# Kernel tuning notes

Measured on AMD Instinct MI355X. Metric: run time of the kernel, lower is better.

The kernel has to match this reference:

```python
import jax, jax.numpy as jnp
import numpy as np

ARRAY_SIZE = 128   # crossbar rows
CBITS = 4          # psum ADC bits
LEV = 2 ** (CBITS - 1)
ALPHA = ARRAY_SIZE / LEV   # psum quant step
EPS = 1e-5

# ---- binary activation / weight quant with STE (hardtanh grad) ----
@jax.custom_vjp
def ste_sign(x):
    return jnp.where(x >= 0, 1.0, -1.0).astype(x.dtype)

def _sign_fwd(x):
    return ste_sign(x), x

def _sign_bwd(x, g):
    return (g * (jnp.abs(x) <= 1.0).astype(g.dtype),)

ste_sign.defvjp(_sign_fwd, _sign_bwd)

# ---- psum (partial-sum) quantization: cbits-level ADC over each crossbar array ----
@jax.custom_vjp
def psum_quant(p):
    return jnp.clip(jnp.round(p / ALPHA), -LEV, LEV - 1) * ALPHA

def _pq_fwd(p):
    return psum_quant(p), p

def _pq_bwd(p, g):
    return (g * (jnp.abs(p) <= ARRAY_SIZE).astype(g.dtype),)

psum_quant.defvjp(_pq_fwd, _pq_bwd)

# ---- layers ----
def bn(x, p):
    g, b, m, v = p  # each [C]
    sh = (1, -1) + (1,) * (x.ndim - 2)
    return (x - m.reshape(sh)) * (g.reshape(sh) / jnp.sqrt(v.reshape(sh) + EPS)) + b.reshape(sh)

def maxpool2(x):
    return jax.lax.reduce_window(x, -jnp.inf, jax.lax.max, (1, 1, 2, 2), (1, 1, 2, 2), 'VALID')

def conv_same(x, w):
    return jax.lax.conv_general_dilated(x, w, (1, 1), 'SAME')

def psum_conv(x, w):
    # crossbar-mapped conv: input channels split into groups of arraySize//(kh*kw),
    # each group conv'd separately, psum-quantized (ADC), then accumulated.
    O, Cin, kh, kw = w.shape
    chunk = max(1, ARRAY_SIZE // (kh * kw))
    G = -(-Cin // chunk)
    pad = G * chunk - Cin
    xp = jnp.pad(x, ((0, 0), (0, pad), (0, 0), (0, 0)))
    wp = jnp.pad(w, ((0, 0), (0, pad), (0, 0), (0, 0)))
    B, _, H, W = x.shape
    xg = xp.reshape(B, G, chunk, H, W).transpose(1, 0, 2, 3, 4)   # [G,B,c,H,W]
    wg = wp.reshape(O, G, chunk, kh, kw).transpose(1, 0, 2, 3, 4)  # [G,O,c,kh,kw]
    ps = jax.vmap(conv_same)(xg, wg)                               # [G,B,O,H,W]
    return psum_quant(ps).sum(0)

def psum_linear(x, w):
    # x [B,D], w [O,D]; D divisible by ARRAY_SIZE
    B, D = x.shape
    O = w.shape[0]
    G = D // ARRAY_SIZE
    ps = jnp.einsum('bgc,ogc->gbo', x.reshape(B, G, ARRAY_SIZE), w.reshape(O, G, ARRAY_SIZE))
    return psum_quant(ps).sum(0)


def setup_inputs() -> dict:
    key = jax.random.key(0)
    ks = iter(jax.random.split(key, 64))
    def nrm(shape, s=0.05):
        return jax.random.normal(next(ks), shape, jnp.float32) * s
    def bnp(C):
        return jnp.stack([jax.random.uniform(next(ks), (C,), jnp.float32) + 0.5,
                          nrm((C,), 0.1), nrm((C,), 0.1),
                          jax.random.uniform(next(ks), (C,), jnp.float32) + 0.5])
    return dict(
        x=jax.random.normal(next(ks), (64, 3, 32, 32), jnp.float32),
        conv0_w=nrm((128, 3, 3, 3)), bn0=bnp(128),
        w1=nrm((128, 128, 3, 3)), bn1=bnp(128),
        w2=nrm((256, 128, 3, 3)), bn2=bnp(256),
        w3=nrm((256, 256, 3, 3)), bn3=bnp(256),
        w4=nrm((512, 256, 3, 3)), bn4=bnp(512),
        w5=nrm((512, 512, 3, 3)), bn5=bnp(512),
        fc1_w=nrm((1024, 8192)), bnf1=bnp(1024),
        fc2_w=nrm((1024, 1024)), bnf2=bnp(1024),
        out_w=nrm((10, 1024)), out_b=nrm((10,)), bnout=bnp(10),
    )


def reference(x, conv0_w, bn0, w1, bn1, w2, bn2, w3, bn3, w4, bn4, w5, bn5,
              fc1_w, bnf1, fc2_w, bnf2, out_w, out_b, bnout):
    h = conv_same(x, conv0_w)                       # full-precision first conv
    h = ste_sign(bn(h, bn0))
    h = psum_conv(h, ste_sign(w1)); h = maxpool2(h); h = ste_sign(bn(h, bn1))
    h = psum_conv(h, ste_sign(w2)); h = ste_sign(bn(h, bn2))
    h = psum_conv(h, ste_sign(w3)); h = maxpool2(h); h = ste_sign(bn(h, bn3))
    h = psum_conv(h, ste_sign(w4)); h = ste_sign(bn(h, bn4))
    h = psum_conv(h, ste_sign(w5)); h = maxpool2(h); h = ste_sign(bn(h, bn5))
    h = h.reshape(h.shape[0], -1)                   # [B, 8192]
    h = ste_sign(bn(psum_linear(h, ste_sign(fc1_w)), bnf1))
    h = bn(psum_linear(h, ste_sign(fc2_w)), bnf2)   # abits=32 -> identity nonlinear
    h = h @ out_w.T + out_b
    return bn(h, bnout)
```

## Files before the change

### kernel.cpp

```cpp
#include <hip/hip_runtime.h>
#include <cstdint>
#include <cstddef>

using bf16x8 = __attribute__((ext_vector_type(8))) short;
using f32x4  = __attribute__((ext_vector_type(4))) float;
using u32x4  = __attribute__((ext_vector_type(4))) unsigned int;

#define DI __device__ __forceinline__

DI float pq3(float a) {
    return fminf(rintf(a), 7.f);
}
DI float pq16(float ps) {
    return fminf(rintf(ps * 0.0625f), 7.f) * 16.f;
}

DI float bnv(float x, float g, float b, float m, float v) {
    return (x - m) * (g / sqrtf(v + 1e-5f)) + b;
}

DI unsigned short sgn_bf16(float v) {
    return (v >= 0.f) ? (unsigned short)0x3F80 : (unsigned short)0xBF80;
}

__global__ __launch_bounds__(256)
void k_conv0(const float* __restrict__ x, const float* __restrict__ w,
             const float* __restrict__ bnp, unsigned short* __restrict__ out) {
    __shared__ float sX[3][3][36];
    const int b = blockIdx.x >> 5, y = blockIdx.x & 31;
    const int tid = threadIdx.x;
    const int o = tid & 127, xc = tid >> 7;

    for (int i = tid; i < 3 * 3 * 36; i += 256) {
        int col = i % 36, rr = (i / 36) % 3, c = i / 108;
        int gy = y + rr - 1, gx = col - 1;
        float v = 0.f;
        if ((unsigned)gy < 32u && (unsigned)gx < 32u)
            v = x[((b * 3 + c) * 32 + gy) * 32 + gx];
        sX[c][rr][col] = v;
    }
    float wr[27];
    const float* wp = w + o * 27;
    #pragma unroll
    for (int t = 0; t < 27; ++t) wr[t] = wp[t];
    __syncthreads();

    const float bg = bnp[o], bb = bnp[128 + o], bm = bnp[256 + o], bv = bnp[384 + o];
    unsigned short* op = out + ((size_t)(b * 32 + y) * 32) * 128 + o;

    #pragma unroll
    for (int q = 0; q < 4; ++q) {
        float acc0 = 0.f, acc1 = 0.f, acc2 = 0.f, acc3 = 0.f;
        const int X0 = xc * 16 + q * 4;
        #pragma unroll
        for (int c = 0; c < 3; ++c)
            #pragma unroll
            for (int ky = 0; ky < 3; ++ky) {
                float xv0 = sX[c][ky][X0 + 0], xv1 = sX[c][ky][X0 + 1];
                float xv2 = sX[c][ky][X0 + 2], xv3 = sX[c][ky][X0 + 3];
                float xv4 = sX[c][ky][X0 + 4], xv5 = sX[c][ky][X0 + 5];
                float w0 = wr[c * 9 + ky * 3 + 0];
                float w1 = wr[c * 9 + ky * 3 + 1];
                float w2 = wr[c * 9 + ky * 3 + 2];
                acc0 += xv0 * w0 + xv1 * w1 + xv2 * w2;
                acc1 += xv1 * w0 + xv2 * w1 + xv3 * w2;
                acc2 += xv2 * w0 + xv3 * w1 + xv4 * w2;
                acc3 += xv3 * w0 + xv4 * w1 + xv5 * w2;
            }
        op[(size_t)(X0 + 0) * 128] = sgn_bf16(bnv(acc0, bg, bb, bm, bv));
        op[(size_t)(X0 + 1) * 128] = sgn_bf16(bnv(acc1, bg, bb, bm, bv));
        op[(size_t)(X0 + 2) * 128] = sgn_bf16(bnv(acc2, bg, bb, bm, bv));
        op[(size_t)(X0 + 3) * 128] = sgn_bf16(bnv(acc3, bg, bb, bm, bv));
    }
}

__global__ __launch_bounds__(256)
void k_pack_w2(const float* __restrict__ w, unsigned short* __restrict__ wpk,
               int Cin, int O, int G) {
    int idx = blockIdx.x * 256 + threadIdx.x;
    if (idx >= G * O * 160) return;
    int c8 = idx & 7;
    int o  = (idx >> 3) % O;
    int r2 = (idx >> 3) / O;
    int chdw = r2 & 1, tap = (r2 >> 1) % 10, g = r2 / 20;
    int c = chdw * 8 + c8, cg = g * 14 + c;
    unsigned short v = 0;
    if (tap < 9 && c < 14 && cg < Cin)
        v = (w[((size_t)o * Cin + cg) * 9 + tap] >= 0.f) ? (unsigned short)0x3D80
                                                         : (unsigned short)0xBD80;
    wpk[idx] = v;
}

template <int H, int W, int Cin, int O, int G, int RH, int RW, int POOLMODE, int OT>
__global__ __launch_bounds__(256)
void k_conv_mfma(const unsigned int* __restrict__ act,
                 const char* __restrict__ wpk2,
                 const float* __restrict__ bnp,
                 unsigned short* __restrict__ outa,
                 unsigned short* __restrict__ a5p,
                 const unsigned int* __restrict__ zbuf) {
    constexpr int SH = RH + 2, SW = RW + 2;
    constexpr int MS = RH * RW / 16;
    constexpr int NREGX = W / RW;
    constexpr int SLOT8 = SH * SW * 8;
    constexpr int NST = (SLOT8 + 255) / 256;
    constexpr int NHF = OT / 32;
    static_assert(MS == 4, "2x2 decomposition needs MS==4");
    static_assert(OT == 64 || OT == 32, "OT must be 64 or 32");
    static_assert(POOLMODE != 1 || RW == 16, "pool mode 1 needs RW=16");
    static_assert(POOLMODE != 2 || RW == 8, "pool mode 2 needs 8x8");

    __shared__ __align__(16) unsigned int sA[SH * SW * 12];

    const int tid  = threadIdx.x;
    const int regY = (int)blockIdx.x / NREGX, regX = (int)blockIdx.x % NREGX;
    const int o0   = blockIdx.y * OT;
    const int b    = blockIdx.z;

    const int lane = tid & 63, wv = tid >> 6;
    const int n  = lane & 15;
    const int kb = lane >> 4;
    const int hb = kb >> 1, ch = kb & 1;
    const int mp = wv & 1;
    const int oh = wv >> 1;

    const unsigned int* sptr[NST];
    int sdst[NST];
    #pragma unroll
    for (int it = 0; it < NST; ++it) {
        int i = it * 256 + tid;
        sdst[it] = -1;
        if (i < SLOT8) {
            int cp = i & 7, slot = i >> 3;
            int yy = slot / SW, xx = slot - yy * SW;
            int gy = regY * RH + yy - 1, gx = regX * RW + xx - 1;
            sdst[it] = slot * 12 + (((cp >> 2) + slot) % 3) * 4 + (cp & 3);
            sptr[it] = ((unsigned)gy < (unsigned)H && (unsigned)gx < (unsigned)W)
                     ? act + ((size_t)(b * H + gy) * W + gx) * (Cin / 2) + cp
                     : zbuf + cp;
        }
    }

    int offMS[2][5];
    #pragma unroll
    for (int j = 0; j < 2; ++j) {
        int p = (2 * mp + j) * 16 + n;
        int y = p / RW, x = p % RW;
        #pragma unroll
        for (int s = 0; s < 5; ++s) {
            int t = 2 * s + hb;
            int slotT = (t <= 8) ? ((y + t / 3) * SW + (x + t % 3)) : (y * SW + x);
            offMS[j][s] = slotT * 48 + ((ch + slotT) % 3) * 16;
        }
    }

    float tot[2][NHF][4];
    #pragma unroll
    for (int j = 0; j < 2; ++j)
        #pragma unroll
        for (int hf = 0; hf < NHF; ++hf)
            #pragma unroll
            for (int r = 0; r < 4; ++r) tot[j][hf][r] = 0.f;

    const char* wl = wpk2 + (size_t)(o0 + oh * (OT / 2) + n) * 16 + (size_t)ch * (O * 16);

    #pragma unroll 1
    for (int g = 0; g < G; ++g) {
        #pragma unroll
        for (int it = 0; it < NST; ++it)
            if (sdst[it] >= 0) {
                sA[sdst[it]] = *sptr[it];
                sptr[it] += 7;
            }
        bf16x8 bq[NHF][5];
        #pragma unroll
        for (int s = 0; s < 5; ++s) {
            const char* wt = wl + (size_t)(2 * s + hb) * (2 * O * 16);
            #pragma unroll
            for (int hf = 0; hf < NHF; ++hf)
                bq[hf][s] = *(const bf16x8*)(wt + hf * 256);
        }
        wl += (size_t)20 * O * 16;
        __syncthreads();

        const char* sAc = (const char*)sA;
        #pragma unroll
        for (int j = 0; j < 2; ++j) {
            f32x4 acc[NHF];
            #pragma unroll
            for (int hf = 0; hf < NHF; ++hf) acc[hf] = (f32x4){0.f, 0.f, 0.f, 0.f};
            #pragma unroll
            for (int s = 0; s < 5; ++s) {
                bf16x8 af = *(const bf16x8*)(sAc + offMS[j][s]);
                #pragma unroll
                for (int hf = 0; hf < NHF; ++hf)
                    acc[hf] = __builtin_amdgcn_mfma_f32_16x16x32_bf16(af, bq[hf][s], acc[hf], 0, 0, 0);
            }
            #pragma unroll
            for (int hf = 0; hf < NHF; ++hf)
                #pragma unroll
                for (int r = 0; r < 4; ++r)
                    tot[j][hf][r] += pq3(acc[hf][r]);
        }
        __syncthreads();
    }

    #pragma unroll
    for (int hf = 0; hf < NHF; ++hf) {
        const int oc = o0 + oh * (OT / 2) + hf * 16 + n;
        const float bg = bnp[oc], bb = bnp[O + oc], bm = bnp[2 * O + oc], bvr = bnp[3 * O + oc];

        if constexpr (POOLMODE == 0) {
            #pragma unroll
            for (int j = 0; j < 2; ++j)
                #pragma unroll
                for (int r = 0; r < 4; ++r) {
                    int p = (2 * mp + j) * 16 + 4 * kb + r;
                    int y = regY * RH + p / RW, x = regX * RW + p % RW;
                    float val = bnv(16.f * tot[j][hf][r], bg, bb, bm, bvr);
                    outa[(((size_t)b * H + y) * W + x) * O + oc] = sgn_bf16(val);
                }
        } else if constexpr (POOLMODE == 1) {
            #pragma unroll
            for (int q = 0; q < 2; ++q) {
                float v = fmaxf(fmaxf(tot[0][hf][2 * q], tot[0][hf][2 * q + 1]),
                                fmaxf(tot[1][hf][2 * q], tot[1][hf][2 * q + 1]));
                float val = bnv(16.f * v, bg, bb, bm, bvr);
                int py = regY * (RH / 2) + mp, px = regX * (RW / 2) + 2 * kb + q;
                outa[(((size_t)b * (H / 2) + py) * (W / 2) + px) * O + oc] = sgn_bf16(val);
            }
        } else {
            #pragma unroll
            for (int j = 0; j < 2; ++j)
                #pragma unroll
                for (int q = 0; q < 2; ++q) {
                    float h = fmaxf(tot[j][hf][2 * q], tot[j][hf][2 * q + 1]);
                    float o2 = __shfl_xor(h, 32);
                    float v = fmaxf(h, o2);
                    if (hb == 0) {
                        float val = bnv(16.f * v, bg, bb, bm, bvr);
                        int d = oc * 16 + (2 * mp + j) * 4 + 2 * ch + q;
                        a5p[((size_t)(d >> 3) * 64 + b) * 8 + (d & 7)] = sgn_bf16(val);
                    }
                }
        }
    }
}

template <int D, int GPB>
__global__ __launch_bounds__(256)
void k_fc_mfma(const unsigned short* __restrict__ bpk, const float* __restrict__ w,
               float* __restrict__ accg) {
    const int lane = threadIdx.x & 63, wv = threadIdx.x >> 6;
    const int n = lane & 15, kb = lane >> 4;
    const int orow = blockIdx.x * 64 + wv * 16 + n;
    const int g0 = blockIdx.y * GPB;

    float tot[4][4];
    #pragma unroll
    for (int s = 0; s < 4; ++s)
        #pragma unroll
        for (int r = 0; r < 4; ++r) tot[s][r] = 0.f;

    #pragma unroll 1
    for (int g = 0; g < GPB; ++g) {
        const int kbase = (g0 + g) * 128;
        f32x4 a0 = {0,0,0,0}, a1 = {0,0,0,0}, a2 = {0,0,0,0}, a3 = {0,0,0,0};
        #pragma unroll
        for (int s = 0; s < 4; ++s) {
            const int k0 = kbase + s * 32 + kb * 8;
            const float* wp = w + (size_t)orow * D + k0;
            float4 wlo = *(const float4*)wp;
            float4 whi = *(const float4*)(wp + 4);
            bf16x8 af;
            af[0] = (short)sgn_bf16(wlo.x); af[1] = (short)sgn_bf16(wlo.y);
            af[2] = (short)sgn_bf16(wlo.z); af[3] = (short)sgn_bf16(wlo.w);
            af[4] = (short)sgn_bf16(whi.x); af[5] = (short)sgn_bf16(whi.y);
            af[6] = (short)sgn_bf16(whi.z); af[7] = (short)sgn_bf16(whi.w);
            const unsigned short* bp = bpk + (size_t)(k0 >> 3) * 512;
            bf16x8 b0 = *(const bf16x8*)(bp + (n +  0) * 8);
            bf16x8 b1 = *(const bf16x8*)(bp + (n + 16) * 8);
            bf16x8 b2 = *(const bf16x8*)(bp + (n + 32) * 8);
            bf16x8 b3 = *(const bf16x8*)(bp + (n + 48) * 8);
            a0 = __builtin_amdgcn_mfma_f32_16x16x32_bf16(af, b0, a0, 0, 0, 0);
            a1 = __builtin_amdgcn_mfma_f32_16x16x32_bf16(af, b1, a1, 0, 0, 0);
            a2 = __builtin_amdgcn_mfma_f32_16x16x32_bf16(af, b2, a2, 0, 0, 0);
            a3 = __builtin_amdgcn_mfma_f32_16x16x32_bf16(af, b3, a3, 0, 0, 0);
        }
        #pragma unroll
        for (int r = 0; r < 4; ++r) {
            tot[0][r] += pq16(a0[r]); tot[1][r] += pq16(a1[r]);
            tot[2][r] += pq16(a2[r]); tot[3][r] += pq16(a3[r]);
        }
    }
    const int od = blockIdx.x * 64 + wv * 16 + kb * 4;
    #pragma unroll
    for (int s = 0; s < 4; ++s)
        #pragma unroll
        for (int r = 0; r < 4; ++r)
            atomicAdd(&accg[(size_t)(od + r) * 64 + s * 16 + n], tot[s][r]);
}

template <bool SIGN>
__global__ __launch_bounds__(256)
void k_fc_ep(const float* __restrict__ accg, const float* __restrict__ bnp,
             unsigned short* __restrict__ packed, float* __restrict__ h2, int O) {
    int idx = blockIdx.x * 256 + threadIdx.x;
    int b = idx & 63, o = idx >> 6;
    float val = bnv(accg[idx], bnp[o], bnp[O + o], bnp[2 * O + o], bnp[3 * O + o]);
    if (SIGN) packed[((size_t)(o >> 3) * 64 + b) * 8 + (o & 7)] = sgn_bf16(val);
    else      h2[(size_t)b * 1024 + o] = val;
}

__global__ __launch_bounds__(64)
void k_out(const float* __restrict__ h2, const float* __restrict__ ow,
           const float* __restrict__ ob, const float* __restrict__ bnp,
           float* __restrict__ out) {
    int b = blockIdx.x / 10, o = blockIdx.x % 10;
    int lane = threadIdx.x;
    float acc = 0.f;
    #pragma unroll
    for (int i = 0; i < 16; ++i) {
        int k = i * 64 + lane;
        acc += h2[b * 1024 + k] * ow[o * 1024 + k];
    }
    #pragma unroll
    for (int off = 32; off; off >>= 1) acc += __shfl_xor(acc, off);
    if (lane == 0)
        out[b * 10 + o] = bnv(acc + ob[o], bnp[o], bnp[10 + o], bnp[20 + o], bnp[30 + o]);
}

extern "C" void kernel_launch(void* const* d_in, const int* in_sizes, int n_in,
                              void* d_out, int out_size, void* d_ws, size_t ws_size,
                              hipStream_t stream) {
    const float* x     = (const float*)d_in[0];
    const float* w0    = (const float*)d_in[1];
    const float* bn0   = (const float*)d_in[2];
    const float* w1    = (const float*)d_in[3];
    const float* bn1   = (const float*)d_in[4];
    const float* w2    = (const float*)d_in[5];
    const float* bn2   = (const float*)d_in[6];
    const float* w3    = (const float*)d_in[7];
    const float* bn3   = (const float*)d_in[8];
    const float* w4    = (const float*)d_in[9];
    const float* bn4   = (const float*)d_in[10];
    const float* w5    = (const float*)d_in[11];
    const float* bn5   = (const float*)d_in[12];
    const float* fc1w  = (const float*)d_in[13];
    const float* bnf1  = (const float*)d_in[14];
    const float* fc2w  = (const float*)d_in[15];
    const float* bnf2  = (const float*)d_in[16];
    const float* outw  = (const float*)d_in[17];
    const float* outb  = (const float*)d_in[18];
    const float* bnout = (const float*)d_in[19];

    char* ws = (char*)d_ws;
    unsigned short* actA  = (unsigned short*)(ws);
    unsigned short* actB  = (unsigned short*)(ws + 16777216);
    unsigned short* wpk   = (unsigned short*)(ws + 20971520);
    unsigned short* a5p   = (unsigned short*)(ws + 27262976);
    unsigned short* a6p   = (unsigned short*)(ws + 28311552);
    float*          h1acc = (float*)(ws + 28442624);
    float*          h2acc = (float*)(ws + 28704768);
    float*          h2    = (float*)(ws + 28966912);
    unsigned int*   zbuf  = (unsigned int*)(ws + 29229056);

    const unsigned int* actA32 = (const unsigned int*)actA;
    const unsigned int* actB32 = (const unsigned int*)actB;
    const char* wpkc = (const char*)wpk;

    hipMemsetAsync(h1acc, 0, 262144, stream);
    hipMemsetAsync(h2acc, 0, 262144, stream);
    hipMemsetAsync(zbuf, 0, 4096, stream);

    k_conv0<<<dim3(2048), dim3(256), 0, stream>>>(x, w0, bn0, actA);

    k_pack_w2<<<dim3(800), dim3(256), 0, stream>>>(w1, wpk, 128, 128, 10);
    k_conv_mfma<32, 32, 128, 128, 10, 4, 16, 1, 64>
        <<<dim3(16, 2, 64), dim3(256), 0, stream>>>(actA32, wpkc, bn1, actB, nullptr, zbuf);

    k_pack_w2<<<dim3(1600), dim3(256), 0, stream>>>(w2, wpk, 128, 256, 10);
    k_conv_mfma<16, 16, 128, 256, 10, 4, 16, 0, 64>
        <<<dim3(4, 4, 64), dim3(256), 0, stream>>>(actB32, wpkc, bn2, actA, nullptr, zbuf);

    k_pack_w2<<<dim3(3040), dim3(256), 0, stream>>>(w3, wpk, 256, 256, 19);
    k_conv_mfma<16, 16, 256, 256, 19, 4, 16, 1, 64>
        <<<dim3(4, 4, 64), dim3(256), 0, stream>>>(actA32, wpkc, bn3, actB, nullptr, zbuf);

    k_pack_w2<<<dim3(6080), dim3(256), 0, stream>>>(w4, wpk, 256, 512, 19);
    k_conv_mfma<8, 8, 256, 512, 19, 8, 8, 0, 32>
        <<<dim3(1, 16, 64), dim3(256), 0, stream>>>(actB32, wpkc, bn4, actA, nullptr, zbuf);

    k_pack_w2<<<dim3(11840), dim3(256), 0, stream>>>(w5, wpk, 512, 512, 37);
    k_conv_mfma<8, 8, 512, 512, 37, 8, 8, 2, 32>
        <<<dim3(1, 16, 64), dim3(256), 0, stream>>>(actA32, wpkc, bn5, nullptr, a5p, zbuf);

    k_fc_mfma<8192, 1><<<dim3(16, 64), dim3(256), 0, stream>>>(a5p, fc1w, h1acc);
    k_fc_ep<true><<<dim3(256), dim3(256), 0, stream>>>(h1acc, bnf1, a6p, nullptr, 1024);
    k_fc_mfma<1024, 1><<<dim3(16, 8), dim3(256), 0, stream>>>(a6p, fc2w, h2acc);
    k_fc_ep<false><<<dim3(256), dim3(256), 0, stream>>>(h2acc, bnf2, nullptr, h2, 1024);
    k_out<<<dim3(640), dim3(64), 0, stream>>>(h2, outw, outb, bnout, (float*)d_out);
}
```

Baseline: 265.2 us.

## Pad activation channels to 16-per-group layout for vectorized conv staging

Activations are now written with each 14-channel crossbar group padded to 16 channels (cidx14 mapping, padded row strides of 160, 304 and 592). Each thread can then stage a full half-group with a single 16-byte load instead of several strided 32-bit loads. The LDS tile shrinks from 12 to 10 words per slot, and the intermediate buffers are remapped to fit the larger padded activations. The trade-off is more activation memory traffic. The pad channels are never written, so the result depends on them holding finite values, since they are multiplied by zero weights.

```diff
diff --git a/kernel.cpp b/kernel.cpp
--- a/kernel.cpp
+++ b/kernel.cpp
@@ -22,6 +22,8 @@
 DI unsigned short sgn_bf16(float v) {
     return (v >= 0.f) ? (unsigned short)0x3F80 : (unsigned short)0xBF80;
 }
+
+DI int cidx14(int oc) { return oc + 2 * (oc / 14); }
 
 __global__ __launch_bounds__(256)
 void k_conv0(const float* __restrict__ x, const float* __restrict__ w,
@@ -46,7 +48,7 @@
     __syncthreads();
 
     const float bg = bnp[o], bb = bnp[128 + o], bm = bnp[256 + o], bv = bnp[384 + o];
-    unsigned short* op = out + ((size_t)(b * 32 + y) * 32) * 128 + o;
+    unsigned short* op = out + (size_t)((b * 32 + y) * 32) * 160 + cidx14(o);
 
     #pragma unroll
     for (int q = 0; q < 4; ++q) {
@@ -67,10 +69,10 @@
                 acc2 += xv2 * w0 + xv3 * w1 + xv4 * w2;
                 acc3 += xv3 * w0 + xv4 * w1 + xv5 * w2;
             }
-        op[(size_t)(X0 + 0) * 128] = sgn_bf16(bnv(acc0, bg, bb, bm, bv));
-        op[(size_t)(X0 + 1) * 128] = sgn_bf16(bnv(acc1, bg, bb, bm, bv));
-        op[(size_t)(X0 + 2) * 128] = sgn_bf16(bnv(acc2, bg, bb, bm, bv));
-        op[(size_t)(X0 + 3) * 128] = sgn_bf16(bnv(acc3, bg, bb, bm, bv));
+        op[(size_t)(X0 + 0) * 160] = sgn_bf16(bnv(acc0, bg, bb, bm, bv));
+        op[(size_t)(X0 + 1) * 160] = sgn_bf16(bnv(acc1, bg, bb, bm, bv));
+        op[(size_t)(X0 + 2) * 160] = sgn_bf16(bnv(acc2, bg, bb, bm, bv));
+        op[(size_t)(X0 + 3) * 160] = sgn_bf16(bnv(acc3, bg, bb, bm, bv));
     }
 }
 
@@ -91,7 +93,8 @@
     wpk[idx] = v;
 }
 
-template <int H, int W, int Cin, int O, int G, int RH, int RW, int POOLMODE, int OT>
+template <int H, int W, int CPAD, int O, int G, int RH, int RW, int POOLMODE,
+          int OT, int PADCOUT>
 __global__ __launch_bounds__(256)
 void k_conv_mfma(const unsigned int* __restrict__ act,
                  const char* __restrict__ wpk2,
@@ -102,15 +105,15 @@
     constexpr int SH = RH + 2, SW = RW + 2;
     constexpr int MS = RH * RW / 16;
     constexpr int NREGX = W / RW;
-    constexpr int SLOT8 = SH * SW * 8;
-    constexpr int NST = (SLOT8 + 255) / 256;
+    constexpr int NV = SH * SW * 2;
     constexpr int NHF = OT / 32;
     static_assert(MS == 4, "2x2 decomposition needs MS==4");
+    static_assert(NV <= 256, "one stage op per thread");
     static_assert(OT == 64 || OT == 32, "OT must be 64 or 32");
     static_assert(POOLMODE != 1 || RW == 16, "pool mode 1 needs RW=16");
     static_assert(POOLMODE != 2 || RW == 8, "pool mode 2 needs 8x8");
 
-    __shared__ __align__(16) unsigned int sA[SH * SW * 12];
+    __shared__ __align__(16) unsigned int sA[SH * SW * 10];
 
     const int tid  = threadIdx.x;
     const int regY = (int)blockIdx.x / NREGX, regX = (int)blockIdx.x % NREGX;
@@ -124,21 +127,16 @@
     const int mp = wv & 1;
     const int oh = wv >> 1;
 
-    const unsigned int* sptr[NST];
-    int sdst[NST];
-    #pragma unroll
-    for (int it = 0; it < NST; ++it) {
-        int i = it * 256 + tid;
-        sdst[it] = -1;
-        if (i < SLOT8) {
-            int cp = i & 7, slot = i >> 3;
-            int yy = slot / SW, xx = slot - yy * SW;
-            int gy = regY * RH + yy - 1, gx = regX * RW + xx - 1;
-            sdst[it] = slot * 12 + (((cp >> 2) + slot) % 3) * 4 + (cp & 3);
-            sptr[it] = ((unsigned)gy < (unsigned)H && (unsigned)gx < (unsigned)W)
-                     ? act + ((size_t)(b * H + gy) * W + gx) * (Cin / 2) + cp
-                     : zbuf + cp;
-        }
+    const unsigned int* sptr = zbuf;
+    int sdst = -1;
+    if (tid < NV) {
+        int c = tid & 1, slot = tid >> 1;
+        int yy = slot / SW, xx = slot - yy * SW;
+        int gy = regY * RH + yy - 1, gx = regX * RW + xx - 1;
+        sdst = slot * 10 + ((c + slot) & 1) * 4;
+        sptr = ((unsigned)gy < (unsigned)H && (unsigned)gx < (unsigned)W)
+             ? act + ((size_t)(b * H + gy) * W + gx) * (CPAD / 2) + c * 4
+             : zbuf + c * 4;
     }
 
     int offMS[2][5];
@@ -150,7 +148,7 @@
         for (int s = 0; s < 5; ++s) {
             int t = 2 * s + hb;
             int slotT = (t <= 8) ? ((y + t / 3) * SW + (x + t % 3)) : (y * SW + x);
-            offMS[j][s] = slotT * 48 + ((ch + slotT) % 3) * 16;
+            offMS[j][s] = slotT * 40 + ((ch + slotT) & 1) * 16;
         }
     }
 
@@ -166,12 +164,10 @@
 
     #pragma unroll 1
     for (int g = 0; g < G; ++g) {
-        #pragma unroll
-        for (int it = 0; it < NST; ++it)
-            if (sdst[it] >= 0) {
-                sA[sdst[it]] = *sptr[it];
-                sptr[it] += 7;
-            }
+        if (sdst >= 0) {
+            *(u32x4*)&sA[sdst] = *(const u32x4*)sptr;
+            sptr += 8;
+        }
         bf16x8 bq[NHF][5];
         #pragma unroll
         for (int s = 0; s < 5; ++s) {
@@ -211,6 +207,7 @@
         const float bg = bnp[oc], bb = bnp[O + oc], bm = bnp[2 * O + oc], bvr = bnp[3 * O + oc];
 
         if constexpr (POOLMODE == 0) {
+            const int co = cidx14(oc);
             #pragma unroll
             for (int j = 0; j < 2; ++j)
                 #pragma unroll
@@ -218,16 +215,17 @@
                     int p = (2 * mp + j) * 16 + 4 * kb + r;
                     int y = regY * RH + p / RW, x = regX * RW + p % RW;
                     float val = bnv(16.f * tot[j][hf][r], bg, bb, bm, bvr);
-                    outa[(((size_t)b * H + y) * W + x) * O + oc] = sgn_bf16(val);
+                    outa[(((size_t)b * H + y) * W + x) * PADCOUT + co] = sgn_bf16(val);
                 }
         } else if constexpr (POOLMODE == 1) {
+            const int co = cidx14(oc);
             #pragma unroll
             for (int q = 0; q < 2; ++q) {
                 float v = fmaxf(fmaxf(tot[0][hf][2 * q], tot[0][hf][2 * q + 1]),
                                 fmaxf(tot[1][hf][2 * q], tot[1][hf][2 * q + 1]));
                 float val = bnv(16.f * v, bg, bb, bm, bvr);
                 int py = regY * (RH / 2) + mp, px = regX * (RW / 2) + 2 * kb + q;
-                outa[(((size_t)b * (H / 2) + py) * (W / 2) + px) * O + oc] = sgn_bf16(val);
+                outa[(((size_t)b * (H / 2) + py) * (W / 2) + px) * PADCOUT + co] = sgn_bf16(val);
             }
         } else {
             #pragma unroll
@@ -356,17 +354,19 @@
 
     char* ws = (char*)d_ws;
     unsigned short* actA  = (unsigned short*)(ws);
-    unsigned short* actB  = (unsigned short*)(ws + 16777216);
-    unsigned short* wpk   = (unsigned short*)(ws + 20971520);
-    unsigned short* a5p   = (unsigned short*)(ws + 27262976);
-    unsigned short* a6p   = (unsigned short*)(ws + 28311552);
-    float*          h1acc = (float*)(ws + 28442624);
-    float*          h2acc = (float*)(ws + 28704768);
-    float*          h2    = (float*)(ws + 28966912);
-    unsigned int*   zbuf  = (unsigned int*)(ws + 29229056);
-
-    const unsigned int* actA32 = (const unsigned int*)actA;
-    const unsigned int* actB32 = (const unsigned int*)actB;
+    unsigned short* actB  = (unsigned short*)(ws + 20971520);
+    unsigned short* actC  = (unsigned short*)(ws + 26214400);
+    unsigned short* wpk   = (unsigned short*)(ws + 36175872);
+    unsigned short* a5p   = (unsigned short*)(ws + 42467328);
+    unsigned short* a6p   = (unsigned short*)(ws + 43515904);
+    float*          h1acc = (float*)(ws + 43646976);
+    float*          h2acc = (float*)(ws + 43909120);
+    float*          h2    = (float*)(ws + 44171264);
+    unsigned int*   zbuf  = (unsigned int*)(ws + 44433408);
+
+    unsigned short* actD = actA;
+    unsigned short* actE = actB;
+
     const char* wpkc = (const char*)wpk;
 
     hipMemsetAsync(h1acc, 0, 262144, stream);
@@ -376,24 +376,24 @@
     k_conv0<<<dim3(2048), dim3(256), 0, stream>>>(x, w0, bn0, actA);
 
     k_pack_w2<<<dim3(800), dim3(256), 0, stream>>>(w1, wpk, 128, 128, 10);
-    k_conv_mfma<32, 32, 128, 128, 10, 4, 16, 1, 64>
-        <<<dim3(16, 2, 64), dim3(256), 0, stream>>>(actA32, wpkc, bn1, actB, nullptr, zbuf);
+    k_conv_mfma<32, 32, 160, 128, 10, 4, 16, 1, 64, 160>
+        <<<dim3(16, 2, 64), dim3(256), 0, stream>>>((const unsigned int*)actA, wpkc, bn1, actB, nullptr, zbuf);
 
     k_pack_w2<<<dim3(1600), dim3(256), 0, stream>>>(w2, wpk, 128, 256, 10);
-    k_conv_mfma<16, 16, 128, 256, 10, 4, 16, 0, 64>
-        <<<dim3(4, 4, 64), dim3(256), 0, stream>>>(actB32, wpkc, bn2, actA, nullptr, zbuf);
+    k_conv_mfma<16, 16, 160, 256, 10, 4, 16, 0, 64, 304>
+        <<<dim3(4, 4, 64), dim3(256), 0, stream>>>((const unsigned int*)actB, wpkc, bn2, actC, nullptr, zbuf);
 
     k_pack_w2<<<dim3(3040), dim3(256), 0, stream>>>(w3, wpk, 256, 256, 19);
-    k_conv_mfma<16, 16, 256, 256, 19, 4, 16, 1, 64>
-        <<<dim3(4, 4, 64), dim3(256), 0, stream>>>(actA32, wpkc, bn3, actB, nullptr, zbuf);
+    k_conv_mfma<16, 16, 304, 256, 19, 4, 16, 1, 64, 304>
+        <<<dim3(4, 4, 64), dim3(256), 0, stream>>>((const unsigned int*)actC, wpkc, bn3, actD, nullptr, zbuf);
 
     k_pack_w2<<<dim3(6080), dim3(256), 0, stream>>>(w4, wpk, 256, 512, 19);
-    k_conv_mfma<8, 8, 256, 512, 19, 8, 8, 0, 32>
-        <<<dim3(1, 16, 64), dim3(256), 0, stream>>>(actB32, wpkc, bn4, actA, nullptr, zbuf);
+    k_conv_mfma<8, 8, 304, 512, 19, 8, 8, 0, 32, 592>
+        <<<dim3(1, 16, 64), dim3(256), 0, stream>>>((const unsigned int*)actD, wpkc, bn4, actE, nullptr, zbuf);
 
     k_pack_w2<<<dim3(11840), dim3(256), 0, stream>>>(w5, wpk, 512, 512, 37);
-    k_conv_mfma<8, 8, 512, 512, 37, 8, 8, 2, 32>
-        <<<dim3(1, 16, 64), dim3(256), 0, stream>>>(actA32, wpkc, bn5, nullptr, a5p, zbuf);
+    k_conv_mfma<8, 8, 592, 512, 37, 8, 8, 2, 32, 0>
+        <<<dim3(1, 16, 64), dim3(256), 0, stream>>>((const unsigned int*)actE, wpkc, bn5, nullptr, a5p, zbuf);
 
     k_fc_mfma<8192, 1><<<dim3(16, 64), dim3(256), 0, stream>>>(a5p, fc1w, h1acc);
     k_fc_ep<true><<<dim3(256), dim3(256), 0, stream>>>(h1acc, bnf1, a6p, nullptr, 1024);
```

Result: slower. 585.0 us (+120.6%).
